# Performance work log

Hardware: AMD Instinct MI355X
Metric: run time of the kernel (lower is better)

## Reference

```python
import jax, jax.numpy as jnp
import numpy as np

N = 100_000      # nodes
E = 1_600_000    # directed edges (before self-loops)
F_IN = 256       # input node features
H = 128          # hidden_dim
HEADS = 2
C_HEAD = H // HEADS  # 64, GATConv out_channels per head
G = 128          # graphs in batch
NCLS = 10
NEG_SLOPE = 0.2  # PyG GATConv default


def setup_inputs() -> dict:
    key = jax.random.key(0)
    ks = jax.random.split(key, 20)
    p = lambda k, shape: (jax.random.normal(k, shape, jnp.float32) * 0.05)
    x = jax.random.normal(ks[0], (N, F_IN), jnp.float32)
    edge_index = jax.random.randint(ks[1], (2, E), 0, N, dtype=jnp.int64)
    batch = jnp.sort(jax.random.randint(ks[2], (N,), 0, G, dtype=jnp.int64))
    return dict(
        x=x, edge_index=edge_index, batch=batch,
        pre_w=p(ks[3], (F_IN, H)), pre_b=p(ks[4], (H,)),
        w1=p(ks[5], (H, H)), asrc1=p(ks[6], (HEADS, C_HEAD)), adst1=p(ks[7], (HEADS, C_HEAD)), b1=p(ks[8], (H,)),
        w2=p(ks[9], (H, H)), asrc2=p(ks[10], (HEADS, C_HEAD)), adst2=p(ks[11], (HEADS, C_HEAD)), b2=p(ks[12], (H,)),
        post_w1=p(ks[13], (H, H)), post_b1=p(ks[14], (H,)),
        post_w2=p(ks[15], (H, NCLS)), post_b2=p(ks[16], (NCLS,)),
    )


def _gat_conv(h_in, w, a_src, a_dst, b, src, dst):
    # h: [N, heads, c]
    h = (h_in @ w).reshape(N, HEADS, C_HEAD)
    alpha_src = jnp.sum(h * a_src, axis=-1)  # [N, heads]
    alpha_dst = jnp.sum(h * a_dst, axis=-1)  # [N, heads]
    e = jax.nn.leaky_relu(alpha_src[src] + alpha_dst[dst], NEG_SLOPE)  # [E+N, heads]
    # numerically stable softmax over incoming edges of each destination node
    m = jax.ops.segment_max(e, dst, num_segments=N)
    ex = jnp.exp(e - m[dst])
    denom = jax.ops.segment_sum(ex, dst, num_segments=N)
    alpha = ex / denom[dst]                                           # [E+N, heads]
    out = jax.ops.segment_sum(h[src] * alpha[:, :, None], dst, num_segments=N)
    return out.reshape(N, H) + b  # concat heads + bias


def reference(x, edge_index, batch, pre_w, pre_b,
              w1, asrc1, adst1, b1, w2, asrc2, adst2, b2,
              post_w1, post_b1, post_w2, post_b2):
    # PyG GATConv default add_self_loops=True
    loop = jnp.arange(N, dtype=edge_index.dtype)
    src = jnp.concatenate([edge_index[0], loop])
    dst = jnp.concatenate([edge_index[1], loop])

    h = jax.nn.relu(x @ pre_w + pre_b)
    reprs = jax.ops.segment_sum(h, batch, num_segments=G)
    h = jax.nn.relu(_gat_conv(h, w1, asrc1, adst1, b1, src, dst))
    reprs = reprs + jax.ops.segment_sum(h, batch, num_segments=G)
    h = jax.nn.relu(_gat_conv(h, w2, asrc2, adst2, b2, src, dst))
    reprs = reprs + jax.ops.segment_sum(h, batch, num_segments=G)
    z = jax.nn.relu(reprs @ post_w1 + post_b1) @ post_w2 + post_b2
    return jax.nn.log_softmax(z, axis=-1)
```

## Files before the change

### kernel.cpp

```cpp
#include <hip/hip_runtime.h>
#include <hip/hip_bf16.h>
#include <math.h>

#define NNODES 100000
#define NEDGES 1600000
#define FIN 256
#define HDIM 128
#define NGRAPH 128
#define NCLS 10
#define NEG 0.2f

#define NBUCK 98
#define EPB 4096
#define EBLK ((NEDGES + EPB - 1) / EPB)

typedef short bf8 __attribute__((ext_vector_type(8)));
typedef float f4 __attribute__((ext_vector_type(4)));
typedef float f2v __attribute__((ext_vector_type(2)));

__device__ __forceinline__ float lrelu(float x) { return x > 0.f ? x : NEG * x; }

__device__ __forceinline__ unsigned short f2bf(float f) {
  union { float f; unsigned int u; } v; v.f = f;
  unsigned int r = v.u + 0x7fffu + ((v.u >> 16) & 1u);
  return (unsigned short)(r >> 16);
}
__device__ __forceinline__ float bf2f(unsigned short u) {
  union { unsigned int u; float f; } v; v.u = ((unsigned int)u) << 16; return v.f;
}
__device__ __forceinline__ float fast_rcp(float x) {
  float r;
  asm("v_rcp_f32 %0, %1" : "=v"(r) : "v"(x));
  return r;
}
__device__ __forceinline__ unsigned cvt_pk_bf16(float lo, float hi) {
  unsigned r;
  asm("v_cvt_pk_bf16_f32 %0, %1, %2" : "=v"(r) : "v"(lo), "v"(hi));
  return r;
}
__device__ __forceinline__ unsigned short pk_fp8(float a, float b) {
  return (unsigned short)__builtin_amdgcn_cvt_pk_fp8_f32(a, b, 0, false);
}
__device__ __forceinline__ f2v pk_unpack_fp8(unsigned p) {
#if __has_builtin(__builtin_amdgcn_cvt_pk_f32_fp8)
  return __builtin_amdgcn_cvt_pk_f32_fp8((int)p, false);
#else
  f2v r;
  r.x = __builtin_amdgcn_cvt_f32_fp8(p, 0);
  r.y = __builtin_amdgcn_cvt_f32_fp8(p, 1);
  return r;
#endif
}

__global__ __launch_bounds__(256) void convert_transpose(const float* __restrict__ w,
                                                         unsigned short* __restrict__ wt,
                                                         int K) {
  int i = blockIdx.x * 256 + threadIdx.x;
  if (i >= K * 128) return;
  int k = i >> 7, n = i & 127;
  wt[n * K + k] = f2bf(w[(size_t)k * 128 + n]);
}

__global__ __launch_bounds__(256) void gemm_mfma(const void* __restrict__ Av,
                                                 int a_bf16,
                                                 const unsigned short* __restrict__ Bt,
                                                 const float* __restrict__ bias,
                                                 unsigned short* __restrict__ Cb,
                                                 unsigned short* __restrict__ Cp,
                                                 const float* __restrict__ a_src,
                                                 const float* __restrict__ a_dst,
                                                 float* __restrict__ o_as,
                                                 float* __restrict__ o_ad,
                                                 int M, int K, int dorelu) {
  __shared__ bf8 As[512];
  __shared__ bf8 Bs[512];
  int tid = threadIdx.x;
  int wv = tid >> 6, lane = tid & 63;
  int quad = lane >> 4, m16 = lane & 15;
  int row0 = blockIdx.x * 128;

  int rA0 = row0 + (tid >> 6) * 16 + (lane & 15); if (rA0 > M - 1) rA0 = M - 1;
  int rA1 = rA0 + 64; if (rA1 > M - 1) rA1 = M - 1;
  int nB0 = (tid >> 6) * 16 + (lane & 15);
  int nB1 = (4 + (tid >> 6)) * 16 + (lane & 15);
  int cOff = (lane >> 4) * 8;

  float4 f0a, f0b, f0c, f0d, f1a, f1b, f1c, f1d;
  bf8 h0a, h0b, h1a, h1b, b00, b01, b10, b11;

  auto loadT0 = [&](int kb) {
    if (a_bf16) {
      h0a = *reinterpret_cast<const bf8*>((const unsigned short*)Av + (size_t)rA0 * K + kb + cOff);
      h0b = *reinterpret_cast<const bf8*>((const unsigned short*)Av + (size_t)rA1 * K + kb + cOff);
    } else {
      const float* p0 = (const float*)Av + (size_t)rA0 * K + kb + cOff;
      const float* p1 = (const float*)Av + (size_t)rA1 * K + kb + cOff;
      f0a = *reinterpret_cast<const float4*>(p0);
      f0b = *reinterpret_cast<const float4*>(p0 + 4);
      f0c = *reinterpret_cast<const float4*>(p1);
      f0d = *reinterpret_cast<const float4*>(p1 + 4);
    }
    b00 = *reinterpret_cast<const bf8*>(&Bt[(size_t)nB0 * K + kb + cOff]);
    b01 = *reinterpret_cast<const bf8*>(&Bt[(size_t)nB1 * K + kb + cOff]);
  };
  auto loadT1 = [&](int kb) {
    if (a_bf16) {
      h1a = *reinterpret_cast<const bf8*>((const unsigned short*)Av + (size_t)rA0 * K + kb + cOff);
      h1b = *reinterpret_cast<const bf8*>((const unsigned short*)Av + (size_t)rA1 * K + kb + cOff);
    } else {
      const float* p0 = (const float*)Av + (size_t)rA0 * K + kb + cOff;
      const float* p1 = (const float*)Av + (size_t)rA1 * K + kb + cOff;
      f1a = *reinterpret_cast<const float4*>(p0);
      f1b = *reinterpret_cast<const float4*>(p0 + 4);
      f1c = *reinterpret_cast<const float4*>(p1);
      f1d = *reinterpret_cast<const float4*>(p1 + 4);
    }
    b10 = *reinterpret_cast<const bf8*>(&Bt[(size_t)nB0 * K + kb + cOff]);
    b11 = *reinterpret_cast<const bf8*>(&Bt[(size_t)nB1 * K + kb + cOff]);
  };
  auto cvt8 = [&](float4 a, float4 b) -> bf8 {
    bf8 v;
    v[0] = (short)f2bf(a.x); v[1] = (short)f2bf(a.y);
    v[2] = (short)f2bf(a.z); v[3] = (short)f2bf(a.w);
    v[4] = (short)f2bf(b.x); v[5] = (short)f2bf(b.y);
    v[6] = (short)f2bf(b.z); v[7] = (short)f2bf(b.w);
    return v;
  };

  f4 acc[16];
#pragma unroll
  for (int b = 0; b < 16; ++b) acc[b] = (f4){0.f, 0.f, 0.f, 0.f};

  loadT0(0);
  loadT1(32);
  for (int kb = 0; kb < K; kb += 64) {
    __syncthreads();
    As[tid]       = a_bf16 ? h0a : cvt8(f0a, f0b);
    As[256 + tid] = a_bf16 ? h0b : cvt8(f0c, f0d);
    Bs[tid] = b00; Bs[tid + 256] = b01;
    __syncthreads();
    if (kb + 64 < K) loadT0(kb + 64);
    {
      bf8 af0 = As[wv * 64 + lane];
      bf8 af1 = As[(wv + 4) * 64 + lane];
#pragma unroll
      for (int tn = 0; tn < 8; ++tn) {
        bf8 bfm = Bs[tn * 64 + lane];
        acc[tn]     = __builtin_amdgcn_mfma_f32_16x16x32_bf16(af0, bfm, acc[tn], 0, 0, 0);
        acc[8 + tn] = __builtin_amdgcn_mfma_f32_16x16x32_bf16(af1, bfm, acc[8 + tn], 0, 0, 0);
      }
    }
    __syncthreads();
    As[tid]       = a_bf16 ? h1a : cvt8(f1a, f1b);
    As[256 + tid] = a_bf16 ? h1b : cvt8(f1c, f1d);
    Bs[tid] = b10; Bs[tid + 256] = b11;
    __syncthreads();
    if (kb + 96 < K) loadT1(kb + 96);
    {
      bf8 af0 = As[wv * 64 + lane];
      bf8 af1 = As[(wv + 4) * 64 + lane];
#pragma unroll
      for (int tn = 0; tn < 8; ++tn) {
        bf8 bfm = Bs[tn * 64 + lane];
        acc[tn]     = __builtin_amdgcn_mfma_f32_16x16x32_bf16(af0, bfm, acc[tn], 0, 0, 0);
        acc[8 + tn] = __builtin_amdgcn_mfma_f32_16x16x32_bf16(af1, bfm, acc[8 + tn], 0, 0, 0);
      }
    }
  }

  if (Cp) {
    if (a_src) {
      float aS[8], aD[8];
#pragma unroll
      for (int tn = 0; tn < 4; ++tn) {
        aS[tn]     = a_src[tn * 16 + m16];
        aS[tn + 4] = a_src[64 + tn * 16 + m16];
        aD[tn]     = a_dst[tn * 16 + m16];
        aD[tn + 4] = a_dst[64 + tn * 16 + m16];
      }
#pragma unroll
      for (int mt = 0; mt < 2; ++mt) {
#pragma unroll
        for (int r = 0; r < 4; ++r) {
          int row = row0 + mt * 64 + wv * 16 + quad * 4 + r;
          float ps0 = 0.f, ps1 = 0.f, pd0 = 0.f, pd1 = 0.f;
#pragma unroll
          for (int tn = 0; tn < 4; ++tn) {
            float v0 = acc[mt * 8 + tn][r], v1 = acc[mt * 8 + tn + 4][r];
            ps0 = fmaf(v0, aS[tn], ps0);
            ps1 = fmaf(v1, aS[tn + 4], ps1);
            pd0 = fmaf(v0, aD[tn], pd0);
            pd1 = fmaf(v1, aD[tn + 4], pd1);
          }
#pragma unroll
          for (int o = 8; o; o >>= 1) {
            ps0 += __shfl_xor(ps0, o); ps1 += __shfl_xor(ps1, o);
            pd0 += __shfl_xor(pd0, o); pd1 += __shfl_xor(pd1, o);
          }
          if (m16 == 0 && row < M) {
            o_as[2 * row] = ps0; o_as[2 * row + 1] = ps1;
            o_ad[2 * row] = pd0; o_ad[2 * row + 1] = pd1;
          }
        }
      }
    }
#pragma unroll
    for (int mt = 0; mt < 2; ++mt)
#pragma unroll
      for (int tn = 0; tn < 4; ++tn)
#pragma unroll
        for (int r = 0; r < 4; ++r) {
          int row = row0 + mt * 64 + wv * 16 + quad * 4 + r;
          if (row < M) {
            Cp[(size_t)row * 64 + tn * 16 + m16] =
                pk_fp8(acc[mt * 8 + tn][r], acc[mt * 8 + tn + 4][r]);
          }
        }
  } else {
#pragma unroll
    for (int mt = 0; mt < 2; ++mt)
#pragma unroll
      for (int tn = 0; tn < 8; ++tn) {
        float bv = bias ? bias[tn * 16 + m16] : 0.f;
#pragma unroll
        for (int r = 0; r < 4; ++r) {
          int row = row0 + mt * 64 + wv * 16 + quad * 4 + r;
          if (row < M) {
            float v = acc[mt * 8 + tn][r] + bv;
            if (dorelu) v = fmaxf(v, 0.f);
            Cb[(size_t)row * 128 + tn * 16 + m16] = f2bf(v);
          }
        }
      }
  }
}

__global__ void find_starts(const int* __restrict__ batch, int* __restrict__ gstart) {
  int g = threadIdx.x;
  if (g > NGRAPH) return;
  if (g == NGRAPH) { gstart[g] = NNODES; return; }
  int lo = 0, hi = NNODES;
  while (lo < hi) { int mid = (lo + hi) >> 1; if (batch[mid] < g) lo = mid + 1; else hi = mid; }
  gstart[g] = lo;
}

__global__ __launch_bounds__(256) void bin_count(const int* __restrict__ edst,
                                                 int* __restrict__ blockHist) {
  __shared__ int hist[NBUCK];
  int t = threadIdx.x, blk = blockIdx.x;
  if (t < NBUCK) hist[t] = 0;
  __syncthreads();
  int e0 = blk * EPB;
#pragma unroll
  for (int it = 0; it < EPB / 256; ++it) {
    int e = e0 + it * 256 + t;
    if (e < NEDGES) atomicAdd(&hist[((unsigned)edst[e]) >> 10], 1);
  }
  __syncthreads();
  if (t < NBUCK) blockHist[blk * NBUCK + t] = hist[t];
}

__global__ __launch_bounds__(512) void colscan(const int* __restrict__ blockHist,
                                               int* __restrict__ blockBaseCol,
                                               int* __restrict__ bucket_total) {
  __shared__ int s[512];
  int b = blockIdx.x, t = threadIdx.x;
  int v = (t < EBLK) ? blockHist[t * NBUCK + b] : 0;
  s[t] = v;
  __syncthreads();
  for (int off = 1; off < 512; off <<= 1) {
    int u = (t >= off) ? s[t - off] : 0;
    __syncthreads();
    s[t] += u;
    __syncthreads();
  }
  if (t < EBLK) blockBaseCol[b * EBLK + t] = s[t] - v;
  if (t == 511) bucket_total[b] = s[511];
}

__global__ __launch_bounds__(128) void bscan(const int* __restrict__ bucket_total,
                                             int* __restrict__ bucket_ptr) {
  __shared__ int s[128];
  int t = threadIdx.x;
  int v = (t < NBUCK) ? bucket_total[t] : 0;
  s[t] = v;
  __syncthreads();
  for (int off = 1; off < 128; off <<= 1) {
    int u = (t >= off) ? s[t - off] : 0;
    __syncthreads();
    s[t] += u;
    __syncthreads();
  }
  if (t < NBUCK) bucket_ptr[t] = s[t] - v;
  if (t == 127) bucket_ptr[NBUCK] = s[127];
}

__global__ __launch_bounds__(512) void bin_place(const int* __restrict__ esrc,
                                                 const int* __restrict__ edst,
                                                 const int* __restrict__ blockBaseCol,
                                                 const int* __restrict__ bucket_ptr,
                                                 unsigned* __restrict__ stagingG) {
  __shared__ int hist[NBUCK + 1], lbase[NBUCK + 1], lcur[NBUCK + 1], cbase[NBUCK];
  __shared__ int tmp[128];
  __shared__ uint2 st[EPB];
  int t = threadIdx.x, blk = blockIdx.x;
  if (t < NBUCK + 1) hist[t] = 0;
  __syncthreads();
  int e0 = blk * EPB;
#pragma unroll
  for (int it = 0; it < EPB / 512; ++it) {
    int e = e0 + it * 512 + t;
    int b = NBUCK;
    if (e < NEDGES) b = ((unsigned)edst[e]) >> 10;
    atomicAdd(&hist[b], 1);
  }
  __syncthreads();
  if (t < 128) tmp[t] = (t < NBUCK + 1) ? hist[t] : 0;
  __syncthreads();
  for (int off = 1; off < 128; off <<= 1) {
    int u = 0;
    if (t < 128 && t >= off) u = tmp[t - off];
    __syncthreads();
    if (t < 128) tmp[t] += u;
    __syncthreads();
  }
  if (t < NBUCK + 1) { int ex = tmp[t] - hist[t]; lbase[t] = ex; lcur[t] = ex; }
  if (t < NBUCK) cbase[t] = bucket_ptr[t] + blockBaseCol[t * EBLK + blk];
  __syncthreads();
#pragma unroll
  for (int it = 0; it < EPB / 512; ++it) {
    int e = e0 + it * 512 + t;
    unsigned s = 0, d = 0xFFFFFFFFu;
    if (e < NEDGES) { s = (unsigned)esrc[e]; d = (unsigned)edst[e]; }
    int b = (d == 0xFFFFFFFFu) ? NBUCK : (int)(d >> 10);
    int slot = atomicAdd(&lcur[b], 1);
    st[slot] = make_uint2(s, d);
  }
  __syncthreads();
  for (int i = t; i < EPB; i += 512) {
    uint2 ed = st[i];
    if (ed.y == 0xFFFFFFFFu) continue;
    int b = (int)(ed.y >> 10);
    stagingG[cbase[b] + (i - lbase[b])] = ((ed.y & 1023u) << 17) | ed.x;
  }
}

__global__ __launch_bounds__(1024) void bucket_csr_fused(const unsigned* __restrict__ stagingG,
                                                         const int* __restrict__ bucket_ptr,
                                                         int* __restrict__ row_ptr,
                                                         int* __restrict__ colv) {
  __shared__ int dl[1024];
  __shared__ int cur[1024];
  int b = blockIdx.x, t = threadIdx.x;
  dl[t] = 0;
  __syncthreads();
  int s0 = bucket_ptr[b], s1 = bucket_ptr[b + 1];
  for (int j = s0 + t; j < s1; j += 1024)
    atomicAdd(&dl[stagingG[j] >> 17], 1);
  __syncthreads();
  int myDeg = dl[t];
  for (int off = 1; off < 1024; off <<= 1) {
    int u = (t >= off) ? dl[t - off] : 0;
    __syncthreads();
    dl[t] += u;
    __syncthreads();
  }
  int rp = s0 + dl[t] - myDeg;
  cur[t] = rp;
  int n = (b << 10) + t;
  if (n < NNODES) row_ptr[n] = rp;
  if (n == NNODES - 1) row_ptr[NNODES] = rp + myDeg;
  __syncthreads();
  for (int j = s0 + t; j < s1; j += 1024) {
    unsigned v = stagingG[j];
    int pos = atomicAdd(&cur[v >> 17], 1);
    colv[pos] = (int)(v & 0x1FFFFu);
  }
}

__global__ __launch_bounds__(256) void aggregate(const unsigned short* __restrict__ hwb,
                                                 const float* __restrict__ a_s,
                                                 const float* __restrict__ a_d,
                                                 const int* __restrict__ row_ptr,
                                                 const int* __restrict__ colv,
                                                 const float* __restrict__ bias,
                                                 unsigned short* __restrict__ out) {
  __shared__ float2 wsh[256];
  int i = (blockIdx.x * 256 + threadIdx.x) >> 6;
  int lane = threadIdx.x & 63;
  if (i >= NNODES) return;
  i = __builtin_amdgcn_readfirstlane(i);
  int wbase = (threadIdx.x >> 6) * 64;

  float ad0 = a_d[2 * i], ad1 = a_d[2 * i + 1];
  int start = row_ptr[i], end = row_ptr[i + 1];
  int deg = end - start;
  float ws0 = __expf(lrelu(a_s[2 * i] + ad0));
  float ws1 = __expf(lrelu(a_s[2 * i + 1] + ad1));

  int sl = 0; float w0l = 0.f, w1l = 0.f;
  if (lane < deg) {
    sl = colv[start + lane];
    float2 av = *reinterpret_cast<const float2*>(&a_s[2 * sl]);
    w0l = __expf(lrelu(av.x + ad0));
    w1l = __expf(lrelu(av.y + ad1));
  }
  wsh[wbase + lane] = make_float2(w0l, w1l);
  float d0 = w0l, d1 = w1l;
  for (int o = 32; o; o >>= 1) { d0 += __shfl_xor(d0, o); d1 += __shfl_xor(d1, o); }
  float den0 = d0 + ws0, den1 = d1 + ws1;

  unsigned ps = hwb[(size_t)i * 64 + lane];
  f2v pv = pk_unpack_fp8(ps);
  float acc0 = ws0 * pv.x, acc1 = ws1 * pv.y;

  int dmin = deg < 64 ? deg : 64;
  int t = 0;
#define GSTEP(T)                                                               \
  {                                                                            \
    int s = __builtin_amdgcn_readlane(sl, (T));                                \
    unsigned q = hwb[(size_t)s * 64 + lane];                                   \
    float2 w = wsh[wbase + (T)];                    \
    f2v xv = pk_unpack_fp8(q);                                                 \
    acc0 = fmaf(w.x, xv.x, acc0);                                              \
    acc1 = fmaf(w.y, xv.y, acc1);                                              \
  }
  for (; t + 8 <= dmin; t += 8) {
    GSTEP(t);     GSTEP(t + 1); GSTEP(t + 2); GSTEP(t + 3);
    GSTEP(t + 4); GSTEP(t + 5); GSTEP(t + 6); GSTEP(t + 7);
  }
  for (; t < dmin; ++t) { GSTEP(t); }
#undef GSTEP

  for (int j = start + 64; j < end; ++j) {
    int s = colv[j];
    float2 av = *reinterpret_cast<const float2*>(&a_s[2 * s]);
    float w0 = __expf(lrelu(av.x + ad0));
    float w1 = __expf(lrelu(av.y + ad1));
    den0 += w0; den1 += w1;
    unsigned q = hwb[(size_t)s * 64 + lane];
    f2v xv = pk_unpack_fp8(q);
    acc0 = fmaf(w0, xv.x, acc0);
    acc1 = fmaf(w1, xv.y, acc1);
  }

  float r0 = fast_rcp(den0), r1 = fast_rcp(den1);
  float o0 = fmaxf(acc0 * r0 + bias[lane], 0.f);
  float o1 = fmaxf(acc1 * r1 + bias[64 + lane], 0.f);
  unsigned pk = cvt_pk_bf16(o0, o1);
  out[(size_t)i * 128 + lane]      = (unsigned short)pk;
  out[(size_t)i * 128 + 64 + lane] = (unsigned short)(pk >> 16);
}

#define SEG_CHUNK 128
__global__ __launch_bounds__(128) void seg_sum_fast(const unsigned short* __restrict__ h,
                                                    const int* __restrict__ batch,
                                                    const int* __restrict__ gstart,
                                                    float* __restrict__ reprs) {
  int n0 = blockIdx.x * SEG_CHUNK;
  if (n0 >= NNODES) return;
  int nend = n0 + SEG_CHUNK; if (nend > NNODES) nend = NNODES;
  int tid = threadIdx.x;
  int r = n0;
  while (r < nend) {
    int g = batch[r];
    int segend = gstart[g + 1]; if (segend > nend) segend = nend;
    float a0 = 0.f, a1 = 0.f, a2 = 0.f, a3 = 0.f;
    for (; r + 3 < segend; r += 4) {
      a0 += bf2f(h[(size_t)r * 128 + tid]);
      a1 += bf2f(h[(size_t)(r + 1) * 128 + tid]);
      a2 += bf2f(h[(size_t)(r + 2) * 128 + tid]);
      a3 += bf2f(h[(size_t)(r + 3) * 128 + tid]);
    }
    for (; r < segend; ++r) a0 += bf2f(h[(size_t)r * 128 + tid]);
    atomicAdd(&reprs[g * 128 + tid], (a0 + a1) + (a2 + a3));
  }
}

__global__ __launch_bounds__(128) void head_kernel(const float* __restrict__ reprs,
                                                   const float* __restrict__ pw1,
                                                   const float* __restrict__ pb1,
                                                   const float* __restrict__ pw2,
                                                   const float* __restrict__ pb2,
                                                   float* __restrict__ out) {
  __shared__ float r[128], t1[128], z[NCLS];
  int g = blockIdx.x, tid = threadIdx.x;
  r[tid] = reprs[g * 128 + tid];
  __syncthreads();
  float acc = pb1[tid];
  for (int k = 0; k < 128; ++k) acc = fmaf(r[k], pw1[k * 128 + tid], acc);
  t1[tid] = fmaxf(acc, 0.f);
  __syncthreads();
  if (tid < NCLS) {
    float zz = pb2[tid];
    for (int k = 0; k < 128; ++k) zz = fmaf(t1[k], pw2[k * NCLS + tid], zz);
    z[tid] = zz;
  }
  __syncthreads();
  if (tid == 0) {
    float mx = -1e30f;
    for (int c = 0; c < NCLS; ++c) mx = fmaxf(mx, z[c]);
    float s = 0.f;
    for (int c = 0; c < NCLS; ++c) s += expf(z[c] - mx);
    float ls = logf(s) + mx;
    for (int c = 0; c < NCLS; ++c) out[g * NCLS + c] = z[c] - ls;
  }
}

extern "C" void kernel_launch(void* const* d_in, const int* in_sizes, int n_in,
                              void* d_out, int out_size, void* d_ws, size_t ws_size,
                              hipStream_t stream) {
  const float* x     = (const float*)d_in[0];
  const int*   eidx  = (const int*)d_in[1];
  const int*   batch = (const int*)d_in[2];
  const float* pre_w = (const float*)d_in[3];
  const float* pre_b = (const float*)d_in[4];
  const float* w1    = (const float*)d_in[5];
  const float* asrc1 = (const float*)d_in[6];
  const float* adst1 = (const float*)d_in[7];
  const float* b1    = (const float*)d_in[8];
  const float* w2    = (const float*)d_in[9];
  const float* asrc2 = (const float*)d_in[10];
  const float* adst2 = (const float*)d_in[11];
  const float* b2    = (const float*)d_in[12];
  const float* pw1   = (const float*)d_in[13];
  const float* pb1   = (const float*)d_in[14];
  const float* pw2   = (const float*)d_in[15];
  const float* pb2   = (const float*)d_in[16];
  float* out = (float*)d_out;

  const int* esrc = eidx;
  const int* edst = eidx + NEDGES;

  char* wsp = (char*)d_ws;
  size_t off = 0;
  auto alloc = [&](size_t bytes) -> void* {
    void* p = wsp + off;
    off += (bytes + 255) & ~(size_t)255;
    return p;
  };
  unsigned short* hb  = (unsigned short*)alloc((size_t)NNODES * 128 * 2);
  unsigned short* hwb = (unsigned short*)alloc((size_t)NNODES * 64 * 2);
  float* a_s         = (float*)alloc((size_t)NNODES * 2 * 4);
  float* a_d         = (float*)alloc((size_t)NNODES * 2 * 4);
  float* reprs       = (float*)alloc((size_t)NGRAPH * 128 * 4);
  int* gstart        = (int*)alloc((NGRAPH + 1) * 4);
  int* row_ptr       = (int*)alloc(((size_t)NNODES + 1) * 4);
  int* colv          = (int*)alloc((size_t)NEDGES * 4);
  unsigned short* wt_pre = (unsigned short*)alloc((size_t)128 * FIN * 2);
  unsigned short* wt1    = (unsigned short*)alloc((size_t)128 * HDIM * 2);
  unsigned short* wt2    = (unsigned short*)alloc((size_t)128 * HDIM * 2);
  int* blockHist     = (int*)alloc((size_t)EBLK * NBUCK * 4);
  int* blockBaseCol  = (int*)alloc((size_t)NBUCK * EBLK * 4);
  int* bucket_total  = (int*)alloc(NBUCK * 4);
  int* bucket_ptr    = (int*)alloc((NBUCK + 1) * 4);
  unsigned* stagingG = (unsigned*)alloc((size_t)NEDGES * 4);

  int wb = NNODES / 4;
  int sb = (NNODES + SEG_CHUNK - 1) / SEG_CHUNK;
  int gb = (NNODES + 127) / 128;

  convert_transpose<<<(FIN * 128 + 255) / 256, 256, 0, stream>>>(pre_w, wt_pre, FIN);
  convert_transpose<<<(HDIM * 128 + 255) / 256, 256, 0, stream>>>(w1, wt1, HDIM);
  convert_transpose<<<(HDIM * 128 + 255) / 256, 256, 0, stream>>>(w2, wt2, HDIM);

  hipMemsetAsync(reprs, 0, (size_t)NGRAPH * 128 * 4, stream);
  find_starts<<<1, 256, 0, stream>>>(batch, gstart);

  bin_count<<<EBLK, 256, 0, stream>>>(edst, blockHist);
  colscan<<<NBUCK, 512, 0, stream>>>(blockHist, blockBaseCol, bucket_total);
  bscan<<<1, 128, 0, stream>>>(bucket_total, bucket_ptr);
  bin_place<<<EBLK, 512, 0, stream>>>(esrc, edst, blockBaseCol, bucket_ptr, stagingG);
  bucket_csr_fused<<<NBUCK, 1024, 0, stream>>>(stagingG, bucket_ptr, row_ptr, colv);

  gemm_mfma<<<gb, 256, 0, stream>>>(x, 0, wt_pre, pre_b, hb, nullptr,
                                    nullptr, nullptr, nullptr, nullptr, NNODES, FIN, 1);
  seg_sum_fast<<<sb, 128, 0, stream>>>(hb, batch, gstart, reprs);

  gemm_mfma<<<gb, 256, 0, stream>>>(hb, 1, wt1, nullptr, nullptr, hwb,
                                    asrc1, adst1, a_s, a_d, NNODES, HDIM, 0);
  aggregate<<<wb, 256, 0, stream>>>(hwb, a_s, a_d, row_ptr, colv, b1, hb);
  seg_sum_fast<<<sb, 128, 0, stream>>>(hb, batch, gstart, reprs);

  gemm_mfma<<<gb, 256, 0, stream>>>(hb, 1, wt2, nullptr, nullptr, hwb,
                                    asrc2, adst2, a_s, a_d, NNODES, HDIM, 0);
  aggregate<<<wb, 256, 0, stream>>>(hwb, a_s, a_d, row_ptr, colv, b2, hb);
  seg_sum_fast<<<sb, 128, 0, stream>>>(hb, batch, gstart, reprs);

  head_kernel<<<NGRAPH, 128, 0, stream>>>(reprs, pw1, pb1, pw2, pb2, out);
}
```

Baseline: 474.8 us.

## Stage whole weight chunk in shared memory, load A directly into registers

Restructures the node-feature GEMM so each block copies a full 128-wide K chunk of the transposed weight into a larger shared buffer, with one barrier per chunk. The A operand is now read straight from global memory into MFMA registers instead of going through shared memory. K and the A dtype become template parameters, and fp32-to-bf16 conversion uses a packed convert helper. This removes most barriers and the A shared-memory round trip, but drops the explicit register double-buffering of global loads, so load latency may be exposed.

```diff
diff --git a/kernel.cpp b/kernel.cpp
--- a/kernel.cpp
+++ b/kernel.cpp
@@ -61,8 +61,8 @@
   wt[n * K + k] = f2bf(w[(size_t)k * 128 + n]);
 }
 
-__global__ __launch_bounds__(256) void gemm_mfma(const void* __restrict__ Av,
-                                                 int a_bf16,
+template<int K, int ABF16>
+__global__ __launch_bounds__(256) void gemm_bres(const void* __restrict__ Av,
                                                  const unsigned short* __restrict__ Bt,
                                                  const float* __restrict__ bias,
                                                  unsigned short* __restrict__ Cb,
@@ -71,99 +71,61 @@
                                                  const float* __restrict__ a_dst,
                                                  float* __restrict__ o_as,
                                                  float* __restrict__ o_ad,
-                                                 int M, int K, int dorelu) {
-  __shared__ bf8 As[512];
-  __shared__ bf8 Bs[512];
+                                                 int M, int dorelu) {
+  __shared__ bf8 Bs[2048];
+  constexpr int NCH = K / 128;
   int tid = threadIdx.x;
   int wv = tid >> 6, lane = tid & 63;
   int quad = lane >> 4, m16 = lane & 15;
   int row0 = blockIdx.x * 128;
 
-  int rA0 = row0 + (tid >> 6) * 16 + (lane & 15); if (rA0 > M - 1) rA0 = M - 1;
+  int rA0 = row0 + wv * 16 + m16; if (rA0 > M - 1) rA0 = M - 1;
   int rA1 = rA0 + 64; if (rA1 > M - 1) rA1 = M - 1;
-  int nB0 = (tid >> 6) * 16 + (lane & 15);
-  int nB1 = (4 + (tid >> 6)) * 16 + (lane & 15);
-  int cOff = (lane >> 4) * 8;
-
-  float4 f0a, f0b, f0c, f0d, f1a, f1b, f1c, f1d;
-  bf8 h0a, h0b, h1a, h1b, b00, b01, b10, b11;
-
-  auto loadT0 = [&](int kb) {
-    if (a_bf16) {
-      h0a = *reinterpret_cast<const bf8*>((const unsigned short*)Av + (size_t)rA0 * K + kb + cOff);
-      h0b = *reinterpret_cast<const bf8*>((const unsigned short*)Av + (size_t)rA1 * K + kb + cOff);
-    } else {
-      const float* p0 = (const float*)Av + (size_t)rA0 * K + kb + cOff;
-      const float* p1 = (const float*)Av + (size_t)rA1 * K + kb + cOff;
-      f0a = *reinterpret_cast<const float4*>(p0);
-      f0b = *reinterpret_cast<const float4*>(p0 + 4);
-      f0c = *reinterpret_cast<const float4*>(p1);
-      f0d = *reinterpret_cast<const float4*>(p1 + 4);
+  int cOff = quad * 8;
+
+  auto cvt8 = [&](float4 a, float4 b) -> bf8 {
+    union { bf8 v; unsigned u[4]; } r;
+    r.u[0] = cvt_pk_bf16(a.x, a.y); r.u[1] = cvt_pk_bf16(a.z, a.w);
+    r.u[2] = cvt_pk_bf16(b.x, b.y); r.u[3] = cvt_pk_bf16(b.z, b.w);
+    return r.v;
+  };
+
+  f4 acc[16];
+#pragma unroll
+  for (int b = 0; b < 16; ++b) acc[b] = (f4){0.f, 0.f, 0.f, 0.f};
+
+  for (int ch = 0; ch < NCH; ++ch) {
+    if (ch) __syncthreads();
+#pragma unroll
+    for (int jj = 0; jj < 8; ++jj) {
+      int j = jj * 256 + tid;
+      int n = ((j >> 6) & 7) * 16 + (j & 15);
+      int k = ch * 128 + (j >> 9) * 32 + ((j >> 4) & 3) * 8;
+      Bs[j] = *reinterpret_cast<const bf8*>(&Bt[(size_t)n * K + k]);
     }
-    b00 = *reinterpret_cast<const bf8*>(&Bt[(size_t)nB0 * K + kb + cOff]);
-    b01 = *reinterpret_cast<const bf8*>(&Bt[(size_t)nB1 * K + kb + cOff]);
-  };
-  auto loadT1 = [&](int kb) {
-    if (a_bf16) {
-      h1a = *reinterpret_cast<const bf8*>((const unsigned short*)Av + (size_t)rA0 * K + kb + cOff);
-      h1b = *reinterpret_cast<const bf8*>((const unsigned short*)Av + (size_t)rA1 * K + kb + cOff);
-    } else {
-      const float* p0 = (const float*)Av + (size_t)rA0 * K + kb + cOff;
-      const float* p1 = (const float*)Av + (size_t)rA1 * K + kb + cOff;
-      f1a = *reinterpret_cast<const float4*>(p0);
-      f1b = *reinterpret_cast<const float4*>(p0 + 4);
-      f1c = *reinterpret_cast<const float4*>(p1);
-      f1d = *reinterpret_cast<const float4*>(p1 + 4);
-    }
-    b10 = *reinterpret_cast<const bf8*>(&Bt[(size_t)nB0 * K + kb + cOff]);
-    b11 = *reinterpret_cast<const bf8*>(&Bt[(size_t)nB1 * K + kb + cOff]);
-  };
-  auto cvt8 = [&](float4 a, float4 b) -> bf8 {
-    bf8 v;
-    v[0] = (short)f2bf(a.x); v[1] = (short)f2bf(a.y);
-    v[2] = (short)f2bf(a.z); v[3] = (short)f2bf(a.w);
-    v[4] = (short)f2bf(b.x); v[5] = (short)f2bf(b.y);
-    v[6] = (short)f2bf(b.z); v[7] = (short)f2bf(b.w);
-    return v;
-  };
-
-  f4 acc[16];
-#pragma unroll
-  for (int b = 0; b < 16; ++b) acc[b] = (f4){0.f, 0.f, 0.f, 0.f};
-
-  loadT0(0);
-  loadT1(32);
-  for (int kb = 0; kb < K; kb += 64) {
-    __syncthreads();
-    As[tid]       = a_bf16 ? h0a : cvt8(f0a, f0b);
-    As[256 + tid] = a_bf16 ? h0b : cvt8(f0c, f0d);
-    Bs[tid] = b00; Bs[tid + 256] = b01;
-    __syncthreads();
-    if (kb + 64 < K) loadT0(kb + 64);
-    {
-      bf8 af0 = As[wv * 64 + lane];
-      bf8 af1 = As[(wv + 4) * 64 + lane];
+    __syncthreads();
+#pragma unroll
+    for (int kt = 0; kt < 4; ++kt) {
+      int kb = ch * 128 + kt * 32;
+      bf8 a0, a1;
+      if (ABF16) {
+        a0 = *reinterpret_cast<const bf8*>((const unsigned short*)Av + (size_t)rA0 * K + kb + cOff);
+        a1 = *reinterpret_cast<const bf8*>((const unsigned short*)Av + (size_t)rA1 * K + kb + cOff);
+      } else {
+        const float* p0 = (const float*)Av + (size_t)rA0 * K + kb + cOff;
+        const float* p1 = (const float*)Av + (size_t)rA1 * K + kb + cOff;
+        float4 x0 = *reinterpret_cast<const float4*>(p0);
+        float4 x1 = *reinterpret_cast<const float4*>(p0 + 4);
+        float4 y0 = *reinterpret_cast<const float4*>(p1);
+        float4 y1 = *reinterpret_cast<const float4*>(p1 + 4);
+        a0 = cvt8(x0, x1);
+        a1 = cvt8(y0, y1);
+      }
 #pragma unroll
       for (int tn = 0; tn < 8; ++tn) {
-        bf8 bfm = Bs[tn * 64 + lane];
-        acc[tn]     = __builtin_amdgcn_mfma_f32_16x16x32_bf16(af0, bfm, acc[tn], 0, 0, 0);
-        acc[8 + tn] = __builtin_amdgcn_mfma_f32_16x16x32_bf16(af1, bfm, acc[8 + tn], 0, 0, 0);
-      }
-    }
-    __syncthreads();
-    As[tid]       = a_bf16 ? h1a : cvt8(f1a, f1b);
-    As[256 + tid] = a_bf16 ? h1b : cvt8(f1c, f1d);
-    Bs[tid] = b10; Bs[tid + 256] = b11;
-    __syncthreads();
-    if (kb + 96 < K) loadT1(kb + 96);
-    {
-      bf8 af0 = As[wv * 64 + lane];
-      bf8 af1 = As[(wv + 4) * 64 + lane];
-#pragma unroll
-      for (int tn = 0; tn < 8; ++tn) {
-        bf8 bfm = Bs[tn * 64 + lane];
-        acc[tn]     = __builtin_amdgcn_mfma_f32_16x16x32_bf16(af0, bfm, acc[tn], 0, 0, 0);
-        acc[8 + tn] = __builtin_amdgcn_mfma_f32_16x16x32_bf16(af1, bfm, acc[8 + tn], 0, 0, 0);
+        bf8 bfm = Bs[kt * 512 + tn * 64 + lane];
+        acc[tn]     = __builtin_amdgcn_mfma_f32_16x16x32_bf16(a0, bfm, acc[tn], 0, 0, 0);
+        acc[8 + tn] = __builtin_amdgcn_mfma_f32_16x16x32_bf16(a1, bfm, acc[8 + tn], 0, 0, 0);
       }
     }
   }
@@ -573,17 +535,17 @@
   bin_place<<<EBLK, 512, 0, stream>>>(esrc, edst, blockBaseCol, bucket_ptr, stagingG);
   bucket_csr_fused<<<NBUCK, 1024, 0, stream>>>(stagingG, bucket_ptr, row_ptr, colv);
 
-  gemm_mfma<<<gb, 256, 0, stream>>>(x, 0, wt_pre, pre_b, hb, nullptr,
-                                    nullptr, nullptr, nullptr, nullptr, NNODES, FIN, 1);
+  gemm_bres<FIN, 0><<<gb, 256, 0, stream>>>(x, wt_pre, pre_b, hb, nullptr,
+                                            nullptr, nullptr, nullptr, nullptr, NNODES, 1);
   seg_sum_fast<<<sb, 128, 0, stream>>>(hb, batch, gstart, reprs);
 
-  gemm_mfma<<<gb, 256, 0, stream>>>(hb, 1, wt1, nullptr, nullptr, hwb,
-                                    asrc1, adst1, a_s, a_d, NNODES, HDIM, 0);
+  gemm_bres<HDIM, 1><<<gb, 256, 0, stream>>>(hb, wt1, nullptr, nullptr, hwb,
+                                             asrc1, adst1, a_s, a_d, NNODES, 0);
   aggregate<<<wb, 256, 0, stream>>>(hwb, a_s, a_d, row_ptr, colv, b1, hb);
   seg_sum_fast<<<sb, 128, 0, stream>>>(hb, batch, gstart, reprs);
 
-  gemm_mfma<<<gb, 256, 0, stream>>>(hb, 1, wt2, nullptr, nullptr, hwb,
-                                    asrc2, adst2, a_s, a_d, NNODES, HDIM, 0);
+  gemm_bres<HDIM, 1><<<gb, 256, 0, stream>>>(hb, wt2, nullptr, nullptr, hwb,
+                                             asrc2, adst2, a_s, a_d, NNODES, 0);
   aggregate<<<wb, 256, 0, stream>>>(hwb, a_s, a_d, row_ptr, colv, b2, hb);
   seg_sum_fast<<<sb, 128, 0, stream>>>(hb, batch, gstart, reprs);
 
```

New measurement: 479.6 us. About the same (+1.0%).
